# Performance work log

Hardware: AMD Instinct MI355X
Metric: run time of the kernel (lower is better)

## Reference

```python
import jax, jax.numpy as jnp
import numpy as np

NH = 50000; NO = 50000; E = 500000; D = 256; L = 8; B = 512; C = 117


def setup_inputs() -> dict:
    key = jax.random.key(0)
    ks = jax.random.split(key, 32)
    s = 0.05
    inp = {
        'x_human': jax.random.normal(ks[0], (NH, D), jnp.float32),
        'x_object': jax.random.normal(ks[1], (NO, D), jnp.float32),
        'edge_index_ho': jax.random.randint(ks[2], (2, E), 0, NH),
        'edge_index_oh': jax.random.randint(ks[3], (2, E), 0, NO),
        'edge_attr_ho': jax.random.normal(ks[4], (E, 2), jnp.float32),
        'edge_attr_oh': jax.random.normal(ks[5], (E, 2), jnp.float32),
        'hbatch': jnp.sort(jax.random.randint(ks[6], (NH,), 0, B)),
        'obatch': jnp.sort(jax.random.randint(ks[7], (NO,), 0, B)),
    }
    # GATConv params per relation, stacked over L layers
    names = ['Wsrc', 'Wdst', 'asrc', 'adst', 'Wedge', 'aedge', 'bias']
    shapes = [(L, D, D), (L, D, D), (L, D), (L, D), (L, 2, D), (L, D), (L, D)]
    i = 8
    for rel in ['ho', 'oh']:
        for n, sh in zip(names, shapes):
            inp[f'{n}_{rel}'] = jax.random.normal(ks[i], sh, jnp.float32) * s
            i += 1
    inp['W_emlp'] = jax.random.normal(ks[i], (2, 32), jnp.float32) * s
    inp['b_emlp'] = jnp.zeros((32,), jnp.float32)
    inp['W_p1'] = jax.random.normal(ks[i + 1], (2 * D + 32, C), jnp.float32) * s
    inp['b_p1'] = jnp.zeros((C,), jnp.float32)
    inp['W_p2'] = jax.random.normal(ks[i + 2], (2 * D + 32, C), jnp.float32) * s
    inp['b_p2'] = jnp.zeros((C,), jnp.float32)
    return inp


def _gat(x_src, x_dst, ei, ea, Wsrc, Wdst, asrc, adst, Wedge, aedge, bias, num_dst):
    # PyG GATConv (heads=1, edge_dim=2, add_self_loops=False)
    h_src = x_src @ Wsrc                       # [Ns, D]
    h_dst = x_dst @ Wdst                       # [Nd, D]
    src, dst = ei[0], ei[1]
    a_s = h_src @ asrc                         # [Ns]
    a_d = h_dst @ adst                         # [Nd]
    a_e = (ea @ Wedge) @ aedge                 # [E]
    logit = jax.nn.leaky_relu(a_s[src] + a_d[dst] + a_e, 0.2)
    m = jax.ops.segment_max(logit, dst, num_segments=num_dst)
    ex = jnp.exp(logit - m[dst])
    denom = jax.ops.segment_sum(ex, dst, num_segments=num_dst)
    alpha = ex / denom[dst]                    # segment softmax over dst
    out = jax.ops.segment_sum(h_src[src] * alpha[:, None], dst, num_segments=num_dst)
    return out + bias


def _seg_mean(x, seg, num):
    s = jax.ops.segment_sum(x, seg, num_segments=num)
    cnt = jax.ops.segment_sum(jnp.ones((x.shape[0],), x.dtype), seg, num_segments=num)
    return s / jnp.maximum(cnt, 1.0)[:, None]


def reference(x_human, x_object, edge_index_ho, edge_index_oh, edge_attr_ho,
              edge_attr_oh, hbatch, obatch,
              Wsrc_ho, Wdst_ho, asrc_ho, adst_ho, Wedge_ho, aedge_ho, bias_ho,
              Wsrc_oh, Wdst_oh, asrc_oh, adst_oh, Wedge_oh, aedge_oh, bias_oh,
              W_emlp, b_emlp, W_p1, b_p1, W_p2, b_p2):
    xh, xo = x_human, x_object
    ph, po = None, None
    for l in range(L):
        nxo = _gat(xh, xo, edge_index_ho, edge_attr_ho, Wsrc_ho[l], Wdst_ho[l],
                   asrc_ho[l], adst_ho[l], Wedge_ho[l], aedge_ho[l], bias_ho[l], NO)
        nxh = _gat(xo, xh, edge_index_oh, edge_attr_oh, Wsrc_oh[l], Wdst_oh[l],
                   asrc_oh[l], adst_oh[l], Wedge_oh[l], aedge_oh[l], bias_oh[l], NH)
        nxh = jax.nn.relu(nxh)
        nxo = jax.nn.relu(nxo)
        if ph is not None:
            nxh = nxh + ph
            nxo = nxo + po
        ph, po = nxh, nxo
        xh, xo = nxh, nxo
    hpool = _seg_mean(xh, hbatch, B)           # [B, D]
    opool = _seg_mean(xo, obatch, B)           # [B, D]
    ea = jax.nn.relu(edge_attr_ho @ W_emlp + b_emlp)  # [E, 32]
    edge_batch = hbatch[edge_index_ho[0]]
    epool = _seg_mean(ea, edge_batch, B)       # [B, 32]
    graph_emb = jnp.concatenate([hpool, opool, epool], axis=-1)  # [B, 544]
    l1 = jax.nn.softmax(graph_emb @ W_p1 + b_p1, axis=1)
    l2 = jax.nn.softmax(graph_emb @ W_p2 + b_p2, axis=1)
    return jnp.stack((l1, l2), axis=1)         # [B, 2, C]
```

## Files before the change

kernel.cpp:

```cpp
#include <hip/hip_runtime.h>
#include <math.h>


#define NNODE 50000
#define EDG   500000
#define DIM   256
#define LAY   8
#define BB    512
#define CC    117
#define EMBD  544
#define SCB   49
#define HW    16384
#define HC    16
#define HNW   4
#define LDSE  4096

typedef short bf16x8 __attribute__((ext_vector_type(8)));
typedef float f32x4  __attribute__((ext_vector_type(4)));

static __device__ __forceinline__ float lrelu(float x){ return x >= 0.f ? x : 0.2f*x; }
static __device__ __forceinline__ unsigned short f2b(float f){
  unsigned int u = __float_as_uint(f);
  unsigned int r = (u + 0x7fffu + ((u >> 16) & 1u)) >> 16;
  return (unsigned short)r;
}
static __device__ __forceinline__ float b2f(unsigned short u){
  return __uint_as_float(((unsigned int)u) << 16);
}
static __device__ __forceinline__ float blo(unsigned int u){
  return __uint_as_float(u << 16);
}
static __device__ __forceinline__ float bhi(unsigned int u){
  return __uint_as_float(u & 0xffff0000u);
}
static __device__ __forceinline__ unsigned cvtpk(float lo, float hi){
  unsigned r;
  asm("v_cvt_pk_bf16_f32 %0, %1, %2" : "=v"(r) : "v"(lo), "v"(hi));
  return r;
}
static __device__ __forceinline__ float rdlane_f(float v, int id){
  return __uint_as_float(__builtin_amdgcn_readlane(__float_as_uint(v), id));
}
static __device__ __forceinline__ int rdlane_i(int v, int id){
  return __builtin_amdgcn_readlane(v, id);
}

static __device__ __forceinline__ void gload_lds16(const void* g, void* l){
  __builtin_amdgcn_global_load_lds((const __attribute__((address_space(1))) void*)g,
                                   (__attribute__((address_space(3))) void*)l,
                                   16, 0, 0);
}

__global__ void vcompute_k(const float* __restrict__ Wsho, const float* __restrict__ Wdho,
                           const float* __restrict__ asho, const float* __restrict__ adho,
                           const float* __restrict__ Wsoh, const float* __restrict__ Wdoh,
                           const float* __restrict__ asoh, const float* __restrict__ adoh,
                           float* __restrict__ vbuf){
  int gid = blockIdx.x*blockDim.x + threadIdx.x;
  int wv = gid >> 6, lane = gid & 63;
  if (wv >= 32*DIM) return;
  int p = wv >> 8, k = wv & 255;
  int which = p & 1, rel = (p>>1)&1, l = p>>2;
  const float* W; const float* a;
  if (rel==0){ W = which? Wdho : Wsho; a = which? adho : asho; }
  else       { W = which? Wdoh : Wsoh; a = which? adoh : asoh; }
  W += (size_t)l*DIM*DIM; a += (size_t)l*DIM;
  const float4* w4 = (const float4*)(W + (size_t)k*DIM);
  const float4* a4 = (const float4*)a;
  float4 wv4 = w4[lane], av4 = a4[lane];
  float s = wv4.x*av4.x + wv4.y*av4.y + wv4.z*av4.z + wv4.w*av4.w;
  for (int off=32; off; off>>=1) s += __shfl_xor(s, off);
  if (lane==0) vbuf[(size_t)p*DIM + k] = s;
}

__global__ void wecompute_k(const float* __restrict__ Weho, const float* __restrict__ aeho,
                            const float* __restrict__ Weoh, const float* __restrict__ aeoh,
                            float* __restrict__ webuf){
  int blk = blockIdx.x;
  int rel = blk & 1, l = blk >> 1;
  const float* We = rel? Weoh : Weho;
  const float* ae = rel? aeoh : aeho;
  int lane = threadIdx.x;
  const float4* w0 = (const float4*)(We + (size_t)l*2*DIM);
  const float4* w1 = (const float4*)(We + (size_t)l*2*DIM + DIM);
  const float4* a4 = (const float4*)(ae + (size_t)l*DIM);
  float4 av = a4[lane], x0 = w0[lane], x1 = w1[lane];
  float s0 = x0.x*av.x + x0.y*av.y + x0.z*av.z + x0.w*av.w;
  float s1 = x1.x*av.x + x1.y*av.y + x1.z*av.z + x1.w*av.w;
  for (int off=32; off; off>>=1){ s0 += __shfl_xor(s0, off); s1 += __shfl_xor(s1, off); }
  if (lane==0){ webuf[blk*2] = s0; webuf[blk*2+1] = s1; }
}

__global__ void histp_k(const int* __restrict__ ei_ho, const int* __restrict__ ei_oh,
                        int* __restrict__ phist){
  __shared__ int h[HW];
  int x = blockIdx.x, y = blockIdx.y, z = blockIdx.z, t = threadIdx.x;
  for (int i=t; i<HW; i+=256) h[i] = 0;
  __syncthreads();
  const int* keys = (z==0)? (ei_ho + EDG) : (z==1)? (ei_oh + EDG) : ei_ho;
  int lo = y << 14;
  int e0 = x * (EDG/HC), e1 = e0 + (EDG/HC);
  for (int e = e0 + t; e < e1; e += 256){
    int k = keys[e] - lo;
    if ((unsigned)k < (unsigned)HW) atomicAdd(&h[k], 1);
  }
  __syncthreads();
  int* dst = phist + (size_t)(((z*HNW + y)*HC + x))*HW;
  for (int i=t; i<HW; i+=256) dst[i] = h[i];
}

static __device__ __forceinline__ int4 phist_sum4(const int* __restrict__ phist,
                                                  int z, int idx){
  int win = idx >> 14, off = idx & (HW-1);
  const int* base = phist + (size_t)((z*HNW + win)*HC)*HW + off;
  int4 s = make_int4(0,0,0,0);
  #pragma unroll
  for (int c=0;c<HC;c++){
    int4 v = *(const int4*)(base + (size_t)c*HW);
    s.x += v.x; s.y += v.y; s.z += v.z; s.w += v.w;
  }
  return s;
}

__global__ void scanA_k(const int* __restrict__ phist, int* __restrict__ bsum){
  __shared__ int sh[256];
  int y = blockIdx.y, b = blockIdx.x, t = threadIdx.x;
  int idx = b*1024 + t*4;
  int s = 0;
  if (idx + 3 < NNODE){
    int4 v = phist_sum4(phist, y, idx);
    s = v.x + v.y + v.z + v.w;
  } else {
    for (int j=0;j<4;j++) if (idx+j < NNODE){
      int win = (idx+j) >> 14, off = (idx+j) & (HW-1);
      for (int c=0;c<HC;c++) s += phist[(size_t)((y*HNW+win)*HC+c)*HW + off];
    }
  }
  sh[t] = s; __syncthreads();
  for (int off=128; off; off>>=1){ if (t<off) sh[t] += sh[t+off]; __syncthreads(); }
  if (t==0) bsum[y*SCB + b] = sh[0];
}

__global__ void scanB_k(int* __restrict__ bsum, int* __restrict__ boff,
                        int* __restrict__ rp0, int* __restrict__ rp1, int* __restrict__ rp2){
  int t = threadIdx.x;
  if (t >= 3) return;
  int run = 0;
  for (int i=0;i<SCB;i++){ boff[t*SCB+i] = run; run += bsum[t*SCB+i]; }
  int* rp = (t==0)? rp0 : (t==1)? rp1 : rp2;
  rp[NNODE] = run;
}

__global__ void scanC_k(const int* __restrict__ phist, const int* __restrict__ boff,
                        int* __restrict__ rp0, int* __restrict__ rp1, int* __restrict__ rp2){
  __shared__ int sh[256];
  int y = blockIdx.y, b = blockIdx.x, t = threadIdx.x;
  int* rp = (y==0)? rp0 : (y==1)? rp1 : rp2;
  int idx = b*1024 + t*4;
  int c[4] = {0,0,0,0};
  if (idx + 3 < NNODE){
    int4 v = phist_sum4(phist, y, idx);
    c[0]=v.x; c[1]=v.y; c[2]=v.z; c[3]=v.w;
  } else {
    for (int j=0;j<4;j++) if (idx+j < NNODE){
      int win = (idx+j) >> 14, off = (idx+j) & (HW-1);
      for (int cc=0;cc<HC;cc++) c[j] += phist[(size_t)((y*HNW+win)*HC+cc)*HW + off];
    }
  }
  int mysum = c[0]+c[1]+c[2]+c[3];
  sh[t] = mysum; __syncthreads();
  for (int off=1; off<256; off<<=1){
    int v = (t>=off) ? sh[t-off] : 0;
    __syncthreads();
    sh[t] += v;
    __syncthreads();
  }
  int base = boff[y*SCB + b] + (sh[t] - mysum);
  int run = 0;
  for (int j=0;j<4;j++){
    if (idx+j < NNODE) rp[idx+j] = base + run;
    run += c[j];
  }
}

__global__ void sxc_k(const float* __restrict__ xh_in, const float* __restrict__ xo_in,
                      unsigned short* __restrict__ xhb, unsigned short* __restrict__ xob,
                      const float* __restrict__ vbuf, float* __restrict__ aset,
                      const int* __restrict__ ei_ho, const int* __restrict__ ei_oh,
                      const float* __restrict__ ea_ho, const float* __restrict__ ea_oh,
                      const int* __restrict__ rp0, const int* __restrict__ rp1,
                      const int* __restrict__ rp2, int* __restrict__ cur,
                      float4* __restrict__ rec0, float4* __restrict__ rec1,
                      float2* __restrict__ eap2){
  int bid = blockIdx.x;
  int y = bid % 5, x = bid / 5;
  if (y < 2){
    int gid = x*blockDim.x + threadIdx.x;
    int w = gid >> 6, lane = gid & 63;
    if (w >= NNODE) return;
    int z = y;
    const float* X = z? xo_in : xh_in;
    unsigned short* O = z? xob : xhb;
    const float* v1 = vbuf + (size_t)(z? 2:0)*DIM;
    const float* v2 = vbuf + (size_t)(z? 1:3)*DIM;
    float* o1 = aset + (size_t)(z? 2:0)*NNODE;
    float* o2 = aset + (size_t)(z? 1:3)*NNODE;
    float4 xv = ((const float4*)(X + (size_t)w*DIM))[lane];
    uint2 ob; ob.x = cvtpk(xv.x, xv.y); ob.y = cvtpk(xv.z, xv.w);
    ((uint2*)O)[(size_t)w*64 + lane] = ob;
    float4 a = ((const float4*)v1)[lane];
    float4 b = ((const float4*)v2)[lane];
    float s1 = xv.x*a.x + xv.y*a.y + xv.z*a.z + xv.w*a.w;
    float s2 = xv.x*b.x + xv.y*b.y + xv.z*b.z + xv.w*b.w;
    for (int off=32; off; off>>=1){ s1 += __shfl_xor(s1, off); s2 += __shfl_xor(s2, off); }
    if (lane==0){ o1[w] = s1; o2[w] = s2; }
  } else {
    int e = x*blockDim.x + threadIdx.x;
    if (e >= EDG) return;
    int yy = y - 2;
    if (yy == 0){
      int d = ei_ho[EDG + e];
      int pos = rp0[d] + atomicAdd(&cur[d], 1);
      rec0[pos] = make_float4(__int_as_float(ei_ho[e]), ea_ho[2*e], ea_ho[2*e+1],
                              __int_as_float(d));
    } else if (yy == 1){
      int d = ei_oh[EDG + e];
      int pos = rp1[d] + atomicAdd(&cur[NNODE + d], 1);
      rec1[pos] = make_float4(__int_as_float(ei_oh[e]), ea_oh[2*e], ea_oh[2*e+1],
                              __int_as_float(d));
    } else {
      int s = ei_ho[e];
      int pos = rp2[s] + atomicAdd(&cur[2*NNODE + s], 1);
      eap2[pos] = make_float2(ea_ho[2*e], ea_ho[2*e+1]);
    }
  }
}

__global__ void wtconv_k(const float* __restrict__ Who, const float* __restrict__ Woh,
                         unsigned short* __restrict__ Wt){
  int gid = blockIdx.x*blockDim.x + threadIdx.x;
  int rel = gid >> 19;
  int rem = gid & ((1<<19)-1);
  int l = rem >> 16;
  int idx = rem & 65535;
  int n = idx >> 8, k = idx & 255;
  const float* W = rel ? Woh : Who;
  Wt[gid] = f2b(W[(size_t)l*65536 + (size_t)k*256 + n]);
}

__global__ __launch_bounds__(256) void gesm_k(
    const unsigned short* __restrict__ A0, const unsigned short* __restrict__ A1,
    const unsigned short* __restrict__ B0, const unsigned short* __restrict__ B1,
    unsigned short* __restrict__ H0, unsigned short* __restrict__ H1, int M,
    const int* __restrict__ rp0, const float4* __restrict__ rec0,
    const int* __restrict__ rp1, const float4* __restrict__ rec1,
    const float* __restrict__ cur_a, const float* __restrict__ wepl,
    uint2* __restrict__ lgsrc0, uint2* __restrict__ lgsrc1){
  union SMu {
    struct { unsigned short As[8192]; unsigned short Bs[8192]; } g;
    float lgs[LDSE];
  };
  __shared__ __align__(16) SMu sh;

  int role = blockIdx.x;
  if (role < 2){
    int z = role;
    const unsigned short* A  = z? A1 : A0;
    const unsigned short* Bt = z? B1 : B0;
    unsigned short* H        = z? H1 : H0;
    int tid = threadIdx.x;
    int col0 = blockIdx.z * 128;
    int row0 = blockIdx.y * 128;
    int w = tid >> 6, lane = tid & 63;
    int q = lane >> 4, ml = lane & 15;
    f32x4 acc[2][8];
    #pragma unroll
    for (int i=0;i<2;i++)
      #pragma unroll
      for (int j=0;j<8;j++) acc[i][j] = (f32x4){0.f,0.f,0.f,0.f};

    const unsigned short* srcA[4];
    const unsigned short* srcB[4];
    #pragma unroll
    for (int p=0;p<4;p++){
      int c = p*256 + w*64 + lane;
      int row = ((c>>7)<<4) | (c&15);
      int sq  = (c>>4)&7;
      int gr = row0 + row; if (gr >= M) gr = M-1;
      srcA[p] = A  + (size_t)gr*256 + sq*8;
      srcB[p] = Bt + (size_t)(col0 + row)*256 + sq*8;
    }

    for (int k0 = 0; k0 < 256; k0 += 64){
      #pragma unroll
      for (int p = 0; p < 4; ++p){
        gload_lds16(srcA[p], &sh.g.As[(size_t)(p*256 + w*64)*8]);
        gload_lds16(srcB[p], &sh.g.Bs[(size_t)(p*256 + w*64)*8]);
        srcA[p] += 64; srcB[p] += 64;
      }
      __syncthreads();
      #pragma unroll
      for (int kk = 0; kk < 2; ++kk){
        bf16x8 a0 = *(const bf16x8*)&sh.g.As[((((2*w+0)*8) + kk*4 + q)*16 + ml)*8];
        bf16x8 a1 = *(const bf16x8*)&sh.g.As[((((2*w+1)*8) + kk*4 + q)*16 + ml)*8];
        #pragma unroll
        for (int nf = 0; nf < 8; ++nf){
          bf16x8 b = *(const bf16x8*)&sh.g.Bs[((nf*8 + kk*4 + q)*16 + ml)*8];
          acc[0][nf] = __builtin_amdgcn_mfma_f32_16x16x32_bf16(a0, b, acc[0][nf], 0,0,0);
          acc[1][nf] = __builtin_amdgcn_mfma_f32_16x16x32_bf16(a1, b, acc[1][nf], 0,0,0);
        }
      }
      __syncthreads();
    }
    #pragma unroll
    for (int mf = 0; mf < 2; ++mf){
      #pragma unroll
      for (int r = 0; r < 4; ++r){
        int gr = row0 + 32*w + 16*mf + q*4 + r;
        if (gr < M){
          #pragma unroll
          for (int nf = 0; nf < 8; ++nf)
            H[(size_t)gr*256 + col0 + nf*16 + ml] = f2b(acc[mf][nf][r]);
        }
      }
    }
  } else {
    int rel = blockIdx.z;
    const int* rp = rel? rp1 : rp0;
    const float4* rec = rel? rec1 : rec0;
    const float* a_s = cur_a + (size_t)(rel? 2:0)*NNODE;
    const float* a_d = cur_a + (size_t)(rel? 3:1)*NNODE;
    float w0 = wepl[rel? 2:0], w1 = wepl[rel? 3:1];
    uint2* lgsrc = rel? lgsrc1 : lgsrc0;
    int n0 = blockIdx.y * 128;
    int n1 = n0 + 128; if (n1 > NNODE) n1 = NNODE;
    int t = threadIdx.x;
    int e0 = rp[n0], e1 = rp[n1];
    bool fit = (e1 - e0) <= LDSE;
    for (int e = e0 + t; e < e1; e += 256){
      float4 r = rec[e];
      int src = __float_as_int(r.x);
      int dst = __float_as_int(r.w);
      float lg = lrelu(a_s[src] + a_d[dst] + r.y*w0 + r.z*w1);
      lgsrc[e] = make_uint2(__float_as_uint(lg), (unsigned)src);
      if (fit) sh.lgs[e - e0] = lg;
    }
    __syncthreads();
    if (t < 128){
      int n = n0 + t;
      if (n < NNODE){
        int st = rp[n], en = rp[n+1];
        float m = -INFINITY, s = 0.f;
        if (fit){
          for (int p=st;p<en;p++) m = fmaxf(m, sh.lgs[p-e0]);
          for (int p=st;p<en;p++) s += __expf(sh.lgs[p-e0] - m);
          float inv = __builtin_amdgcn_rcpf(s);
          for (int p=st;p<en;p++)
            lgsrc[p].x = __float_as_uint(__expf(sh.lgs[p-e0] - m) * inv);
        } else {
          for (int p=st;p<en;p++) m = fmaxf(m, __uint_as_float(lgsrc[p].x));
          for (int p=st;p<en;p++) s += __expf(__uint_as_float(lgsrc[p].x) - m);
          float inv = __builtin_amdgcn_rcpf(s);
          for (int p=st;p<en;p++)
            lgsrc[p].x = __float_as_uint(__expf(__uint_as_float(lgsrc[p].x) - m) * inv);
        }
      }
    }
  }
}

__global__ void attn2_k(const int* __restrict__ rp0, const uint2* __restrict__ lgsrc0,
                        const int* __restrict__ rp1, const uint2* __restrict__ lgsrc1,
                        float* __restrict__ nxt_a,
                        const unsigned short* __restrict__ hs0,
                        const unsigned short* __restrict__ hs1,
                        const float* __restrict__ bias0, const float* __restrict__ bias1,
                        const unsigned short* __restrict__ xprev0,
                        const unsigned short* __restrict__ xprev1,
                        unsigned short* __restrict__ xnext0,
                        unsigned short* __restrict__ xnext1,
                        const float* __restrict__ vbl,
                        int hasRes, int doNext){
  int gid = blockIdx.x*blockDim.x + threadIdx.x;
  int w = gid >> 6, lane = gid & 63;
  if (w >= NNODE) return;
  int rel = blockIdx.y;
  const int* rowptr = rel? rp1 : rp0;
  const uint2* lgsrc = rel? lgsrc1 : lgsrc0;
  const unsigned short* hs = rel? hs1 : hs0;
  const float* bias = rel? bias1 : bias0;
  const unsigned short* xprev = rel? xprev1 : xprev0;
  unsigned short* xnext = rel? xnext1 : xnext0;

  int st = rowptr[w], en = rowptr[w+1];
  int deg = en - st;

  float4 bv = ((const float4*)bias)[lane];
  uint2 rres = ((const uint2*)xprev)[(size_t)w*64 + lane];
  float4 va = ((const float4*)(vbl + (size_t)(rel? 0:2)*DIM))[lane];
  float4 vc = ((const float4*)(vbl + (size_t)(rel? 3:1)*DIM))[lane];

  float ax=0.f, ay=0.f, az=0.f, aw=0.f;
  if (deg > 0 && deg <= 64){
    int sreg = 0; float wgt = 0.f;
    if (lane < deg){
      uint2 ls = lgsrc[st + lane];
      sreg = (int)ls.y;
      wgt = __uint_as_float(ls.x);
    }
    int i = 0;
    for (; i + 7 < deg; i += 8){
      float wi[8]; const uint2* rp[8];
      #pragma unroll
      for (int j=0;j<8;j++){
        wi[j] = rdlane_f(wgt, i+j);
        rp[j] = (const uint2*)(hs + (size_t)rdlane_i(sreg, i+j)*DIM);
      }
      uint2 hv[8];
      #pragma unroll
      for (int j=0;j<8;j++) hv[j] = rp[j][lane];
      #pragma unroll
      for (int j=0;j<8;j++){
        ax += wi[j]*blo(hv[j].x); ay += wi[j]*bhi(hv[j].x);
        az += wi[j]*blo(hv[j].y); aw += wi[j]*bhi(hv[j].y);
      }
    }
    for (; i + 3 < deg; i += 4){
      float wi[4]; const uint2* rp[4];
      #pragma unroll
      for (int j=0;j<4;j++){
        wi[j] = rdlane_f(wgt, i+j);
        rp[j] = (const uint2*)(hs + (size_t)rdlane_i(sreg, i+j)*DIM);
      }
      uint2 hv[4];
      #pragma unroll
      for (int j=0;j<4;j++) hv[j] = rp[j][lane];
      #pragma unroll
      for (int j=0;j<4;j++){
        ax += wi[j]*blo(hv[j].x); ay += wi[j]*bhi(hv[j].x);
        az += wi[j]*blo(hv[j].y); aw += wi[j]*bhi(hv[j].y);
      }
    }
    for (; i < deg; ++i){
      float wi = rdlane_f(wgt, i);
      const uint2* rp = (const uint2*)(hs + (size_t)rdlane_i(sreg, i)*DIM);
      uint2 hv = rp[lane];
      ax += wi*blo(hv.x); ay += wi*bhi(hv.x);
      az += wi*blo(hv.y); aw += wi*bhi(hv.y);
    }
  } else if (deg > 64){
    for (int p = st; p < en; ++p){
      uint2 ls = lgsrc[p];
      float wgt = __uint_as_float(ls.x);
      const uint2* rp = (const uint2*)(hs + (size_t)ls.y*DIM);
      uint2 hv = rp[lane];
      ax += wgt*blo(hv.x); ay += wgt*bhi(hv.x);
      az += wgt*blo(hv.y); aw += wgt*bhi(hv.y);
    }
  }

  float resw = hasRes ? 1.f : 0.f;
  float4 o;
  o.x = fmaxf(ax + bv.x, 0.f) + resw*blo(rres.x);
  o.y = fmaxf(ay + bv.y, 0.f) + resw*bhi(rres.x);
  o.z = fmaxf(az + bv.z, 0.f) + resw*blo(rres.y);
  o.w = fmaxf(aw + bv.w, 0.f) + resw*bhi(rres.y);
  uint2 ob; ob.x = cvtpk(o.x, o.y); ob.y = cvtpk(o.z, o.w);
  ((uint2*)xnext)[(size_t)w*64 + lane] = ob;
  if (doNext){
    float s1 = o.x*va.x + o.y*va.y + o.z*va.z + o.w*va.w;
    float s2 = o.x*vc.x + o.y*vc.y + o.z*vc.z + o.w*vc.w;
    for (int off=32; off; off>>=1){ s1 += __shfl_xor(s1, off); s2 += __shfl_xor(s2, off); }
    if (lane==0){
      float* asn = nxt_a + (size_t)(rel? 0:2)*NNODE;
      float* adn = nxt_a + (size_t)(rel? 3:1)*NNODE;
      asn[w] = s1; adn[w] = s2;
    }
  }
}

__device__ __forceinline__ int lowerb(const int* a, int n, int v){
  int lo=0, hi=n;
  while (lo < hi){ int m = (lo+hi)>>1; if (a[m] < v) lo = m+1; else hi = m; }
  return lo;
}

__global__ void pool2_k(const unsigned short* __restrict__ xh, const unsigned short* __restrict__ xo,
                        const int* __restrict__ hbatch, const int* __restrict__ obatch,
                        float* __restrict__ hpool, float* __restrict__ opool){
  int z = blockIdx.y;
  const unsigned short* x = z? xo : xh;
  const int* batch = z? obatch : hbatch;
  float* out = z? opool : hpool;
  int b = blockIdx.x, t = threadIdx.x;
  int st = lowerb(batch, NNODE, b), en = lowerb(batch, NNODE, b+1);
  float s = 0.f;
  for (int i=st;i<en;i++) s += b2f(x[(size_t)i*DIM + t]);
  out[(size_t)b*DIM + t] = s / fmaxf((float)(en - st), 1.f);
}

__global__ void epool_k(const int* __restrict__ rp_src, const int* __restrict__ hbatch,
                        const float2* __restrict__ eaperm, const float* __restrict__ Wem,
                        const float* __restrict__ bem, float* __restrict__ epool){
  __shared__ float ps[8][33];
  int b = blockIdx.x, t = threadIdx.x;
  int j = t & 31, g = t >> 5;
  int nst = lowerb(hbatch, NNODE, b), nen = lowerb(hbatch, NNODE, b+1);
  int est = rp_src[nst], een = rp_src[nen];
  float w0 = Wem[j], w1 = Wem[32+j], bb = bem[j];
  float s = 0.f;
  for (int p = est + g; p < een; p += 8){
    float2 e = eaperm[p];
    s += fmaxf(e.x*w0 + e.y*w1 + bb, 0.f);
  }
  ps[g][j] = s; __syncthreads();
  if (g == 0){
    float tot = 0.f;
    #pragma unroll
    for (int gg=0; gg<8; gg++) tot += ps[gg][j];
    epool[(size_t)b*32 + j] = tot / fmaxf((float)(een - est), 1.f);
  }
}

__global__ void head_k(const float* __restrict__ hpool, const float* __restrict__ opool,
                       const float* __restrict__ epool,
                       const float* __restrict__ Wp1, const float* __restrict__ bp1,
                       const float* __restrict__ Wp2, const float* __restrict__ bp2,
                       float* __restrict__ out){
  __shared__ float emb[EMBD];
  __shared__ float red[256];
  int b = blockIdx.x, t = threadIdx.x;
  emb[t] = hpool[(size_t)b*DIM + t];
  emb[DIM + t] = opool[(size_t)b*DIM + t];
  if (t < 32) emb[2*DIM + t] = epool[(size_t)b*32 + t];
  __syncthreads();
  for (int h = 0; h < 2; ++h){
    const float* Wp = h? Wp2 : Wp1;
    const float* bp = h? bp2 : bp1;
    float logit = -INFINITY;
    if (t < CC){
      float s = bp[t];
      for (int k=0;k<EMBD;k++) s += emb[k]*Wp[(size_t)k*CC + t];
      logit = s;
    }
    red[t] = logit; __syncthreads();
    for (int off=128; off; off>>=1){ if (t<off) red[t] = fmaxf(red[t], red[t+off]); __syncthreads(); }
    float mx = red[0]; __syncthreads();
    float ex = (t < CC) ? expf(logit - mx) : 0.f;
    red[t] = ex; __syncthreads();
    for (int off=128; off; off>>=1){ if (t<off) red[t] += red[t+off]; __syncthreads(); }
    float sm = red[0]; __syncthreads();
    if (t < CC) out[((size_t)b*2 + h)*CC + t] = ex / sm;
  }
}

extern "C" void kernel_launch(void* const* d_in, const int* in_sizes, int n_in,
                              void* d_out, int out_size, void* d_ws, size_t ws_size,
                              hipStream_t stream) {
  (void)in_sizes; (void)n_in; (void)out_size; (void)ws_size;
  const float* xh_in   = (const float*)d_in[0];
  const float* xo_in   = (const float*)d_in[1];
  const int*   ei_ho   = (const int*)d_in[2];
  const int*   ei_oh   = (const int*)d_in[3];
  const float* ea_ho   = (const float*)d_in[4];
  const float* ea_oh   = (const float*)d_in[5];
  const int*   hbatch  = (const int*)d_in[6];
  const int*   obatch  = (const int*)d_in[7];
  const float* Wsrc_ho = (const float*)d_in[8];
  const float* Wdst_ho = (const float*)d_in[9];
  const float* asrc_ho = (const float*)d_in[10];
  const float* adst_ho = (const float*)d_in[11];
  const float* Wedge_ho= (const float*)d_in[12];
  const float* aedge_ho= (const float*)d_in[13];
  const float* bias_ho = (const float*)d_in[14];
  const float* Wsrc_oh = (const float*)d_in[15];
  const float* Wdst_oh = (const float*)d_in[16];
  const float* asrc_oh = (const float*)d_in[17];
  const float* adst_oh = (const float*)d_in[18];
  const float* Wedge_oh= (const float*)d_in[19];
  const float* aedge_oh= (const float*)d_in[20];
  const float* bias_oh = (const float*)d_in[21];
  const float* W_emlp  = (const float*)d_in[22];
  const float* b_emlp  = (const float*)d_in[23];
  const float* W_p1    = (const float*)d_in[24];
  const float* b_p1    = (const float*)d_in[25];
  const float* W_p2    = (const float*)d_in[26];
  const float* b_p2    = (const float*)d_in[27];
  float* out = (float*)d_out;

  size_t ND = (size_t)NNODE*DIM;
  float* f = (float*)d_ws;
  float* aset0 = f;
  float* aset1 = aset0 + 4*NNODE;
  float* vbuf  = aset1 + 4*NNODE;
  float* webuf = vbuf + 32*DIM;
  float* hpool = webuf + 32;
  float* opool = hpool + (size_t)BB*DIM;
  float* epool = opool + (size_t)BB*DIM;
  float4* rec_ho  = (float4*)(epool + (size_t)BB*32);
  float4* rec_oh  = rec_ho + EDG;
  float2* eap_src = (float2*)(rec_oh + EDG);
  unsigned short* xhb0 = (unsigned short*)(eap_src + EDG);
  unsigned short* xhb1 = xhb0 + ND;
  unsigned short* xob0 = xhb1 + ND;
  unsigned short* xob1 = xob0 + ND;
  unsigned short* hSb0 = xob1 + ND;
  unsigned short* hSb1 = hSb0 + ND;
  unsigned short* Wtb  = hSb1 + ND;
  int* cur     = (int*)(Wtb + (size_t)2*LAY*DIM*DIM);
  int* rp_ho   = cur + 3*NNODE;
  int* rp_oh   = rp_ho + NNODE + 1;
  int* rp_src  = rp_oh + NNODE + 1;
  int* bsum    = rp_src + NNODE + 1;
  int* boff    = bsum + 3*SCB;
  int* phist   = boff + 3*SCB;
  uint2*  lgsrc_ho = (uint2*)phist;
  uint2*  lgsrc_oh = lgsrc_ho + EDG;

  hipMemsetAsync(cur, 0, sizeof(int)*3*NNODE, stream);
  vcompute_k<<<2048, 256, 0, stream>>>(Wsrc_ho, Wdst_ho, asrc_ho, adst_ho,
                                       Wsrc_oh, Wdst_oh, asrc_oh, adst_oh, vbuf);
  wecompute_k<<<16, 64, 0, stream>>>(Wedge_ho, aedge_ho, Wedge_oh, aedge_oh, webuf);
  wtconv_k<<<4096, 256, 0, stream>>>(Wsrc_ho, Wsrc_oh, Wtb);
  histp_k<<<dim3(HC, HNW, 3), 256, 0, stream>>>(ei_ho, ei_oh, phist);
  scanA_k<<<dim3(SCB, 3), 256, 0, stream>>>(phist, bsum);
  scanB_k<<<1, 64, 0, stream>>>(bsum, boff, rp_ho, rp_oh, rp_src);
  scanC_k<<<dim3(SCB, 3), 256, 0, stream>>>(phist, boff, rp_ho, rp_oh, rp_src);
  sxc_k<<<62500, 256, 0, stream>>>(xh_in, xo_in, xhb1, xob1, vbuf, aset0,
                                   ei_ho, ei_oh, ea_ho, ea_oh,
                                   rp_ho, rp_oh, rp_src, cur,
                                   rec_ho, rec_oh, eap_src);

  const unsigned short* xh = xhb1;
  const unsigned short* xo = xob1;
  unsigned short* xh_bufs[2] = {xhb0, xhb1};
  unsigned short* xo_bufs[2] = {xob0, xob1};
  float* asets[2] = {aset0, aset1};
  for (int l = 0; l < LAY; ++l){
    unsigned short* xo_n = xo_bufs[l & 1];
    unsigned short* xh_n = xh_bufs[l & 1];
    float* cur_a = asets[l & 1];
    float* nxt_a = asets[(l & 1) ^ 1];
    int doNext = (l < LAY-1);
    int ln = doNext ? (l+1) : l;
    gesm_k<<<dim3(3, 391, 2), 256, 0, stream>>>(xh, xo,
                                                Wtb + (size_t)l*DIM*DIM,
                                                Wtb + (size_t)(LAY + l)*DIM*DIM,
                                                hSb0, hSb1, NNODE,
                                                rp_ho, rec_ho, rp_oh, rec_oh,
                                                cur_a, webuf + (size_t)l*4,
                                                lgsrc_ho, lgsrc_oh);
    attn2_k<<<dim3(12500, 2), 256, 0, stream>>>(rp_ho, lgsrc_ho,
                                                rp_oh, lgsrc_oh,
                                                nxt_a,
                                                hSb0, hSb1,
                                                bias_ho + (size_t)l*DIM, bias_oh + (size_t)l*DIM,
                                                xo, xh, xo_n, xh_n,
                                                vbuf + (size_t)ln*4*DIM,
                                                l > 0, doNext);
    xh = xh_n; xo = xo_n;
  }

  pool2_k<<<dim3(BB, 2), 256, 0, stream>>>(xh, xo, hbatch, obatch, hpool, opool);
  epool_k<<<BB, 256, 0, stream>>>(rp_src, hbatch, eap_src, W_emlp, b_emlp, epool);
  head_k<<<BB, 256, 0, stream>>>(hpool, opool, epool, W_p1, b_p1, W_p2, b_p2, out);
}
```

Measured before the change: 1.446 ms.

## Parallelize block-sum scan, pad attention tail loop, merge pooling kernels

Replaces the serial three-thread block-offset scan with a wave-level shuffle scan over 192 threads. In the attention aggregation, the scalar remainder loop is folded into a padded 4-wide loop that clamps indices and zeroes weights, giving more loads in flight. The node pooling and edge pooling kernels are merged into one launch to remove a kernel launch. Each piece is small, and the padded loop does redundant loads for low-degree nodes.

```diff
diff --git a/kernel.cpp b/kernel.cpp
--- a/kernel.cpp
+++ b/kernel.cpp
@@ -141,14 +141,23 @@
   if (t==0) bsum[y*SCB + b] = sh[0];
 }
 
-__global__ void scanB_k(int* __restrict__ bsum, int* __restrict__ boff,
+__global__ void scanB_k(const int* __restrict__ bsum, int* __restrict__ boff,
                         int* __restrict__ rp0, int* __restrict__ rp1, int* __restrict__ rp2){
   int t = threadIdx.x;
-  if (t >= 3) return;
-  int run = 0;
-  for (int i=0;i<SCB;i++){ boff[t*SCB+i] = run; run += bsum[t*SCB+i]; }
-  int* rp = (t==0)? rp0 : (t==1)? rp1 : rp2;
-  rp[NNODE] = run;
+  int row = t >> 6, lane = t & 63;
+  if (row >= 3) return;
+  int v = (lane < SCB) ? bsum[row*SCB + lane] : 0;
+  int s = v;
+  for (int off=1; off<64; off<<=1){
+    int u = __shfl_up(s, off);
+    if (lane >= off) s += u;
+  }
+  if (lane < SCB) boff[row*SCB + lane] = s - v;
+  int tot = __shfl(s, SCB-1);
+  if (lane == 0){
+    int* rp = (row==0)? rp0 : (row==1)? rp1 : rp2;
+    rp[NNODE] = tot;
+  }
 }
 
 __global__ void scanC_k(const int* __restrict__ phist, const int* __restrict__ boff,
@@ -425,12 +434,15 @@
         az += wi[j]*blo(hv[j].y); aw += wi[j]*bhi(hv[j].y);
       }
     }
-    for (; i + 3 < deg; i += 4){
+    for (; i < deg; i += 4){
       float wi[4]; const uint2* rp[4];
       #pragma unroll
       for (int j=0;j<4;j++){
-        wi[j] = rdlane_f(wgt, i+j);
-        rp[j] = (const uint2*)(hs + (size_t)rdlane_i(sreg, i+j)*DIM);
+        int id = i + j;
+        int ok = (id < deg);
+        if (!ok) id = deg - 1;
+        wi[j] = ok ? rdlane_f(wgt, id) : 0.f;
+        rp[j] = (const uint2*)(hs + (size_t)rdlane_i(sreg, id)*DIM);
       }
       uint2 hv[4];
       #pragma unroll
@@ -440,13 +452,6 @@
         ax += wi[j]*blo(hv[j].x); ay += wi[j]*bhi(hv[j].x);
         az += wi[j]*blo(hv[j].y); aw += wi[j]*bhi(hv[j].y);
       }
-    }
-    for (; i < deg; ++i){
-      float wi = rdlane_f(wgt, i);
-      const uint2* rp = (const uint2*)(hs + (size_t)rdlane_i(sreg, i)*DIM);
-      uint2 hv = rp[lane];
-      ax += wi*blo(hv.x); ay += wi*bhi(hv.x);
-      az += wi*blo(hv.y); aw += wi*bhi(hv.y);
     }
   } else if (deg > 64){
     for (int p = st; p < en; ++p){
@@ -485,40 +490,40 @@
   return lo;
 }
 
-__global__ void pool2_k(const unsigned short* __restrict__ xh, const unsigned short* __restrict__ xo,
-                        const int* __restrict__ hbatch, const int* __restrict__ obatch,
-                        float* __restrict__ hpool, float* __restrict__ opool){
-  int z = blockIdx.y;
-  const unsigned short* x = z? xo : xh;
-  const int* batch = z? obatch : hbatch;
-  float* out = z? opool : hpool;
+__global__ void poolep_k(const unsigned short* __restrict__ xh, const unsigned short* __restrict__ xo,
+                         const int* __restrict__ hbatch, const int* __restrict__ obatch,
+                         float* __restrict__ hpool, float* __restrict__ opool,
+                         const int* __restrict__ rp_src, const float2* __restrict__ eaperm,
+                         const float* __restrict__ Wem, const float* __restrict__ bem,
+                         float* __restrict__ epool){
+  __shared__ float ps[8][33];
+  int y = blockIdx.y;
   int b = blockIdx.x, t = threadIdx.x;
-  int st = lowerb(batch, NNODE, b), en = lowerb(batch, NNODE, b+1);
-  float s = 0.f;
-  for (int i=st;i<en;i++) s += b2f(x[(size_t)i*DIM + t]);
-  out[(size_t)b*DIM + t] = s / fmaxf((float)(en - st), 1.f);
-}
-
-__global__ void epool_k(const int* __restrict__ rp_src, const int* __restrict__ hbatch,
-                        const float2* __restrict__ eaperm, const float* __restrict__ Wem,
-                        const float* __restrict__ bem, float* __restrict__ epool){
-  __shared__ float ps[8][33];
-  int b = blockIdx.x, t = threadIdx.x;
-  int j = t & 31, g = t >> 5;
-  int nst = lowerb(hbatch, NNODE, b), nen = lowerb(hbatch, NNODE, b+1);
-  int est = rp_src[nst], een = rp_src[nen];
-  float w0 = Wem[j], w1 = Wem[32+j], bb = bem[j];
-  float s = 0.f;
-  for (int p = est + g; p < een; p += 8){
-    float2 e = eaperm[p];
-    s += fmaxf(e.x*w0 + e.y*w1 + bb, 0.f);
-  }
-  ps[g][j] = s; __syncthreads();
-  if (g == 0){
-    float tot = 0.f;
-    #pragma unroll
-    for (int gg=0; gg<8; gg++) tot += ps[gg][j];
-    epool[(size_t)b*32 + j] = tot / fmaxf((float)(een - est), 1.f);
+  if (y < 2){
+    const unsigned short* x = y? xo : xh;
+    const int* batch = y? obatch : hbatch;
+    float* out = y? opool : hpool;
+    int st = lowerb(batch, NNODE, b), en = lowerb(batch, NNODE, b+1);
+    float s = 0.f;
+    for (int i=st;i<en;i++) s += b2f(x[(size_t)i*DIM + t]);
+    out[(size_t)b*DIM + t] = s / fmaxf((float)(en - st), 1.f);
+  } else {
+    int j = t & 31, g = t >> 5;
+    int nst = lowerb(hbatch, NNODE, b), nen = lowerb(hbatch, NNODE, b+1);
+    int est = rp_src[nst], een = rp_src[nen];
+    float w0 = Wem[j], w1 = Wem[32+j], bb = bem[j];
+    float s = 0.f;
+    for (int p = est + g; p < een; p += 8){
+      float2 e = eaperm[p];
+      s += fmaxf(e.x*w0 + e.y*w1 + bb, 0.f);
+    }
+    ps[g][j] = s; __syncthreads();
+    if (g == 0){
+      float tot = 0.f;
+      #pragma unroll
+      for (int gg=0; gg<8; gg++) tot += ps[gg][j];
+      epool[(size_t)b*32 + j] = tot / fmaxf((float)(een - est), 1.f);
+    }
   }
 }
 
@@ -624,7 +629,7 @@
   wtconv_k<<<4096, 256, 0, stream>>>(Wsrc_ho, Wsrc_oh, Wtb);
   histp_k<<<dim3(HC, HNW, 3), 256, 0, stream>>>(ei_ho, ei_oh, phist);
   scanA_k<<<dim3(SCB, 3), 256, 0, stream>>>(phist, bsum);
-  scanB_k<<<1, 64, 0, stream>>>(bsum, boff, rp_ho, rp_oh, rp_src);
+  scanB_k<<<1, 192, 0, stream>>>(bsum, boff, rp_ho, rp_oh, rp_src);
   scanC_k<<<dim3(SCB, 3), 256, 0, stream>>>(phist, boff, rp_ho, rp_oh, rp_src);
   sxc_k<<<62500, 256, 0, stream>>>(xh_in, xo_in, xhb1, xob1, vbuf, aset0,
                                    ei_ho, ei_oh, ea_ho, ea_oh,
@@ -661,7 +666,7 @@
     xh = xh_n; xo = xo_n;
   }
 
-  pool2_k<<<dim3(BB, 2), 256, 0, stream>>>(xh, xo, hbatch, obatch, hpool, opool);
-  epool_k<<<BB, 256, 0, stream>>>(rp_src, hbatch, eap_src, W_emlp, b_emlp, epool);
+  poolep_k<<<dim3(BB, 3), 256, 0, stream>>>(xh, xo, hbatch, obatch, hpool, opool,
+                                            rp_src, eap_src, W_emlp, b_emlp, epool);
   head_k<<<BB, 256, 0, stream>>>(hpool, opool, epool, W_p1, b_p1, W_p2, b_p2, out);
 }
```

New measurement: 1.413 ms, median of 2. -2.3%, faster.
